# Kernel optimization log

Measured on AMD Instinct MI355X. Metric: run time of the kernel, lower is better.

Reference implementation:

```python
import jax, jax.numpy as jnp
import numpy as np

D_MODEL = 1024
HIDDEN = 512
NUM_EXPERTS = 16
TOP_K = 2
CAP_FACTOR = 1.25
ALPHA = 0.01


def setup_inputs() -> dict:
    key = jax.random.key(0)
    ks = jax.random.split(key, 10)
    s_in = 1.0 / np.sqrt(D_MODEL)
    s_h = 1.0 / np.sqrt(HIDDEN)
    return {
        "x": jax.random.normal(ks[0], (4, 4096, D_MODEL), dtype=jnp.float32),
        "gate_w": jax.random.normal(ks[1], (D_MODEL, NUM_EXPERTS), dtype=jnp.float32) * s_in,
        "gate_b": jnp.zeros((NUM_EXPERTS,), dtype=jnp.float32),
        "gp_w": jax.random.normal(ks[2], (NUM_EXPERTS, D_MODEL, HIDDEN), dtype=jnp.float32) * s_in,
        "gp_b": jnp.zeros((NUM_EXPERTS, HIDDEN), dtype=jnp.float32),
        "up_w": jax.random.normal(ks[3], (NUM_EXPERTS, D_MODEL, HIDDEN), dtype=jnp.float32) * s_in,
        "up_b": jnp.zeros((NUM_EXPERTS, HIDDEN), dtype=jnp.float32),
        "dp_w": jax.random.normal(ks[4], (NUM_EXPERTS, HIDDEN, D_MODEL), dtype=jnp.float32) * s_h,
        "dp_b": jnp.zeros((NUM_EXPERTS, D_MODEL), dtype=jnp.float32),
    }


def reference(x, gate_w, gate_b, gp_w, gp_b, up_w, up_b, dp_w, dp_b):
    B, S, D = x.shape
    T = B * S
    xf = x.reshape(T, D)

    # --- MoEGate ---
    logits = xf @ gate_w + gate_b                      # [T, E]
    scores = jax.nn.softmax(logits, axis=-1)
    topk_w, topk_i = jax.lax.top_k(scores, TOP_K)      # [T, K]
    # norm_topk_prob=True in DeepSeekMoE
    topk_w = topk_w / (jnp.sum(topk_w, axis=-1, keepdims=True) + 1e-9)

    one_hot = jax.nn.one_hot(topk_i, NUM_EXPERTS, dtype=jnp.float32)  # [T, K, E]
    load = jnp.sum(one_hot, axis=(0, 1))               # [E]
    capacity = CAP_FACTOR * (T * TOP_K) / NUM_EXPERTS
    capacity_penalty = jnp.sum(jax.nn.relu(load - capacity)) / NUM_EXPERTS / T
    aux_loss = ALPHA * capacity_penalty

    # combine weight of expert e for each token: [T, E]
    comb = jnp.einsum("tke,tk->te", one_hot, topk_w)

    # --- dispatch/combine (dense per-expert, weighted by comb) ---
    out = jnp.zeros_like(xf)
    for e in range(NUM_EXPERTS):
        # Expert: down_proj(gate_proj(x) * silu(up_proj(x)))
        h = (xf @ gp_w[e] + gp_b[e]) * jax.nn.silu(xf @ up_w[e] + up_b[e])
        y = h @ dp_w[e] + dp_b[e]
        out = out + comb[:, e:e + 1] * y

    return out.reshape(B, S, D), aux_loss
```

## Files before the change

### kernel.cpp

```cpp
#include <hip/hip_runtime.h>
#include <hip/hip_bf16.h>
#include <math.h>

#define T_TOK 16384
#define DMODEL 1024
#define HID 512
#define NEXP 16
#define NASSIGN (T_TOK * 2)
#define HIST_BLK 64
#define TOK_PER_BLK (T_TOK / HIST_BLK)
#define NMB_MAX 143

typedef __bf16 bf16_8 __attribute__((ext_vector_type(8)));
typedef __bf16 bf16_4 __attribute__((ext_vector_type(4)));
typedef float f32_4 __attribute__((ext_vector_type(4)));

__device__ __forceinline__ void gload16(const __bf16* g, __bf16* l) {
  __builtin_amdgcn_global_load_lds(
      (const __attribute__((address_space(1))) void*)g,
      (__attribute__((address_space(3))) void*)l, 16, 0, 0);
}

__global__ __launch_bounds__(256) void gate_compute_kernel(
    const float* __restrict__ x, const float* __restrict__ gw, const float* __restrict__ gb,
    __bf16* __restrict__ xb, int* __restrict__ topk_idx, float2* __restrict__ topk_w)
{
  __shared__ __align__(16) float gws[4 * 1024 * 4];

  int tid = threadIdx.x;
#pragma unroll
  for (int i = 0; i < 16; ++i) {
    int c = i * 256 + tid;
    f32_4 v = ((const f32_4*)gw)[c];
    ((f32_4*)gws)[((c & 3) << 10) | (c >> 2)] = v;
  }
  __syncthreads();

  int wave = tid >> 6, lane = tid & 63;
  int tbase = blockIdx.x * 32 + wave * 8;

#pragma unroll 1
  for (int pass = 0; pass < 2; ++pass) {
    int t0 = tbase + pass * 4;
    const float* xr0 = x + (size_t)t0 * DMODEL;
    const float* xr1 = xr0 + DMODEL;
    const float* xr2 = xr1 + DMODEL;
    const float* xr3 = xr2 + DMODEL;
    __bf16* xw0 = xb + (size_t)t0 * DMODEL;
    __bf16* xw1 = xw0 + DMODEL;
    __bf16* xw2 = xw1 + DMODEL;
    __bf16* xw3 = xw2 + DMODEL;

    f32_4 acc0[4], acc1[4], acc2[4], acc3[4];
    {
      f32_4 z = {0.f, 0.f, 0.f, 0.f};
#pragma unroll
      for (int g = 0; g < 4; ++g) { acc0[g] = z; acc1[g] = z; acc2[g] = z; acc3[g] = z; }
    }

#pragma unroll
    for (int j = 0; j < 16; ++j) {
      int k = j * 64 + lane;
      float xv0 = xr0[k], xv1 = xr1[k], xv2 = xr2[k], xv3 = xr3[k];
      xw0[k] = (__bf16)xv0;
      xw1[k] = (__bf16)xv1;
      xw2[k] = (__bf16)xv2;
      xw3[k] = (__bf16)xv3;
      f32_4 w0 = ((const f32_4*)gws)[k];
      f32_4 w1 = ((const f32_4*)gws)[1024 + k];
      f32_4 w2 = ((const f32_4*)gws)[2048 + k];
      f32_4 w3 = ((const f32_4*)gws)[3072 + k];
      acc0[0] += xv0 * w0; acc0[1] += xv0 * w1; acc0[2] += xv0 * w2; acc0[3] += xv0 * w3;
      acc1[0] += xv1 * w0; acc1[1] += xv1 * w1; acc1[2] += xv1 * w2; acc1[3] += xv1 * w3;
      acc2[0] += xv2 * w0; acc2[1] += xv2 * w1; acc2[2] += xv2 * w2; acc2[3] += xv2 * w3;
      acc3[0] += xv3 * w0; acc3[1] += xv3 * w1; acc3[2] += xv3 * w2; acc3[3] += xv3 * w3;
    }

#pragma unroll
    for (int g = 0; g < 4; ++g)
#pragma unroll
      for (int w = 0; w < 4; ++w) {
        float v0 = acc0[g][w], v1 = acc1[g][w], v2 = acc2[g][w], v3 = acc3[g][w];
#pragma unroll
        for (int s = 32; s; s >>= 1) {
          v0 += __shfl_xor(v0, s, 64);
          v1 += __shfl_xor(v1, s, 64);
          v2 += __shfl_xor(v2, s, 64);
          v3 += __shfl_xor(v3, s, 64);
        }
        acc0[g][w] = v0; acc1[g][w] = v1; acc2[g][w] = v2; acc3[g][w] = v3;
      }

    int ti = lane & 3;
    float sc[16];
#pragma unroll
    for (int e = 0; e < 16; ++e) {
      int g = e >> 2, w = e & 3;
      float v = ti == 0 ? acc0[g][w] : ti == 1 ? acc1[g][w] : ti == 2 ? acc2[g][w] : acc3[g][w];
      sc[e] = v + gb[e];
    }
    float mx = -1e30f;
#pragma unroll
    for (int e = 0; e < 16; ++e) mx = fmaxf(mx, sc[e]);
    float Z = 0.f;
#pragma unroll
    for (int e = 0; e < 16; ++e) { sc[e] = expf(sc[e] - mx); Z += sc[e]; }
    int i0 = 0; float s0 = sc[0];
#pragma unroll
    for (int e = 1; e < 16; ++e) if (sc[e] > s0) { s0 = sc[e]; i0 = e; }
    int i1 = -1; float s1 = -1e30f;
#pragma unroll
    for (int e = 0; e < 16; ++e) if (e != i0 && sc[e] > s1) { s1 = sc[e]; i1 = e; }
    s0 /= Z; s1 /= Z;
    float dn = s0 + s1 + 1e-9f;
    if (lane < 4) {
      int t = t0 + ti;
      topk_idx[t] = i0 | (i1 << 8);
      topk_w[t] = make_float2(s0 / dn, s1 / dn);
    }
  }
}

__global__ __launch_bounds__(256) void hist_kernel(
    const int* __restrict__ topk_idx, int* __restrict__ block_hist)
{
  __shared__ int cnt[NEXP];
  int tid = threadIdx.x;
  if (tid < NEXP) cnt[tid] = 0;
  __syncthreads();
  int t = blockIdx.x * TOK_PER_BLK + tid;
  int p = topk_idx[t];
  atomicAdd(&cnt[p & 0xff], 1);
  atomicAdd(&cnt[p >> 8], 1);
  __syncthreads();
  if (tid < NEXP) block_hist[blockIdx.x * NEXP + tid] = cnt[tid];
}

__global__ void scan2_kernel(const int* __restrict__ block_hist,
                             int* __restrict__ counts, int* __restrict__ offsets,
                             int* __restrict__ block_base, int* __restrict__ mb_tab,
                             int* __restrict__ nmb, float* __restrict__ aux_out)
{
  __shared__ int cl[NEXP];
  int lane = threadIdx.x;
  if (lane < NEXP) {
    int s = 0;
    for (int b = 0; b < HIST_BLK; ++b) s += block_hist[b * NEXP + lane];
    cl[lane] = s;
    counts[lane] = s;
  }
  __syncthreads();
  if (lane < NEXP) {
    int off = 0;
    for (int e = 0; e < lane; ++e) off += cl[e];
    offsets[lane] = off;
    int base = off;
    for (int b = 0; b < HIST_BLK; ++b) {
      block_base[b * NEXP + lane] = base;
      base += block_hist[b * NEXP + lane];
    }
  }
  if (lane == 0) {
    int tot = 0; float pen = 0.f;
    const float cap = 1.25f * (float)(T_TOK * 2) / (float)NEXP;
    for (int e = 0; e < NEXP; ++e) {
      tot += cl[e];
      float ld = (float)cl[e] - cap;
      pen += ld > 0.f ? ld : 0.f;
    }
    offsets[NEXP] = tot;
    aux_out[0] = 0.01f * pen / (float)NEXP / (float)T_TOK;
    int idx = 0;
    for (int e = 0; e < NEXP; ++e) {
      int nb = (cl[e] + 255) >> 8;
      for (int b = 0; b < nb; ++b) mb_tab[idx++] = (e << 8) | b;
    }
    nmb[0] = idx;
  }
}

__global__ __launch_bounds__(256) void scatter_kernel(
    const int* __restrict__ topk_idx, const int* __restrict__ block_base,
    int* __restrict__ tok_list, int2* __restrict__ tok_slots)
{
  __shared__ int base[NEXP];
  int tid = threadIdx.x;
  if (tid < NEXP) base[tid] = block_base[blockIdx.x * NEXP + tid];
  __syncthreads();
  int t = blockIdx.x * TOK_PER_BLK + tid;
  int p = topk_idx[t];
  int i0 = p & 0xff, i1 = p >> 8;
  int p0 = atomicAdd(&base[i0], 1);
  tok_list[p0] = t;
  int p1 = atomicAdd(&base[i1], 1);
  tok_list[p1] = t;
  tok_slots[t] = make_int2(p0, p1);
}

__global__ __launch_bounds__(256) void transpose_w1_kernel(const float* __restrict__ gp,
                                                           const float* __restrict__ up,
                                                           __bf16* __restrict__ wb1)
{
  __shared__ float tile[32][33];
  int ez = blockIdx.z;
  int e = ez >> 1, isup = ez & 1;
  const float* in = isup ? up : gp;
  int c0 = blockIdx.x * 32, r0 = blockIdx.y * 32;
  const float* src = in + ((size_t)e * 1024 + r0) * 512 + c0;
#pragma unroll
  for (int i = 0; i < 4; ++i) {
    int r = threadIdx.y + i * 8;
    tile[r][threadIdx.x] = src[(size_t)r * 512 + threadIdx.x];
  }
  __syncthreads();
#pragma unroll
  for (int i = 0; i < 4; ++i) {
    int cc = threadIdx.y + i * 8;
    int np = 2 * c0 + 2 * (cc & ~15) + (cc & 15) + 16 * isup;
    wb1[((size_t)e * 1024 + np) * 1024 + r0 + threadIdx.x] = (__bf16)tile[threadIdx.x][cc];
  }
}

__global__ __launch_bounds__(256) void transpose_dp_kernel(const float* __restrict__ in,
                                                           __bf16* __restrict__ out)
{
  __shared__ float tile[32][33];
  int e = blockIdx.z;
  int c0 = blockIdx.x * 32, r0 = blockIdx.y * 32;
  const float* src = in + ((size_t)e * 512 + r0) * 1024 + c0;
#pragma unroll
  for (int i = 0; i < 4; ++i) {
    int r = threadIdx.y + i * 8;
    tile[r][threadIdx.x] = src[(size_t)r * 1024 + threadIdx.x];
  }
  __syncthreads();
  __bf16* dst = out + ((size_t)e * 1024 + c0) * 512 + r0;
#pragma unroll
  for (int i = 0; i < 4; ++i) {
    int c = threadIdx.y + i * 8;
    dst[(size_t)c * 512 + threadIdx.x] = (__bf16)tile[threadIdx.x][c];
  }
}


#define PHASE_MID()                                          \
  __builtin_amdgcn_sched_barrier(0);                         \
  __builtin_amdgcn_s_barrier();                              \
  asm volatile("s_waitcnt lgkmcnt(0)" ::: "memory");         \
  __builtin_amdgcn_sched_barrier(0);                         \
  __builtin_amdgcn_s_setprio(1);

#define PHASE_END()                                          \
  __builtin_amdgcn_s_setprio(0);                             \
  __builtin_amdgcn_sched_barrier(0);                         \
  __builtin_amdgcn_s_barrier();

#define MF(mi, ni, a, b) acc[mi][ni] = __builtin_amdgcn_mfma_f32_16x16x32_bf16(a, b, acc[mi][ni], 0, 0, 0)

#define STAGE_A(b, kt) {                                       \
    gload16(ga0 + (kt) * 32, lds + (b) * 16384 + tid * 8);     \
    gload16(ga1 + (kt) * 32, lds + (b) * 16384 + 4096 + tid * 8); }
#define STAGE_B(b, kt) {                                       \
    gload16(gb0 + (kt) * 32, lds + (b) * 16384 + 8192 + tid * 8); \
    gload16(gb1 + (kt) * 32, lds + (b) * 16384 + 12288 + tid * 8); }

#define GTILE(ktv, STG, ENDVM)                                                    \
  {                                                                               \
    const __bf16* A_ = lds + ((ktv) & 3) * 16384;                                 \
    const __bf16* B_ = A_ + 8192;                                                 \
    bf16_8 af0, af1, af2, af3, bf0, bf1, bf2, bf3;                                \
    af0 = *(const bf16_8*)(A_ + abase + 0 * 512 + aq);                            \
    af1 = *(const bf16_8*)(A_ + abase + 1 * 512 + aq);                            \
    af2 = *(const bf16_8*)(A_ + abase + 2 * 512 + aq);                            \
    af3 = *(const bf16_8*)(A_ + abase + 3 * 512 + aq);                            \
    bf0 = *(const bf16_8*)(B_ + bbase + 0 * 512 + aq);                            \
    bf1 = *(const bf16_8*)(B_ + bbase + 1 * 512 + aq);                            \
    bf2 = *(const bf16_8*)(B_ + bbase + 2 * 512 + aq);                            \
    bf3 = *(const bf16_8*)(B_ + bbase + 3 * 512 + aq);                            \
    if (STG) STAGE_A(((ktv) + 3) & 3, (ktv) + 3);                                 \
    PHASE_MID();                                                                  \
    MF(0, 0, af0, bf0); MF(0, 1, af0, bf1); MF(0, 2, af0, bf2); MF(0, 3, af0, bf3); \
    MF(1, 0, af1, bf0); MF(1, 1, af1, bf1); MF(1, 2, af1, bf2); MF(1, 3, af1, bf3); \
    MF(2, 0, af2, bf0); MF(2, 1, af2, bf1); MF(2, 2, af2, bf2); MF(2, 3, af2, bf3); \
    MF(3, 0, af3, bf0); MF(3, 1, af3, bf1); MF(3, 2, af3, bf2); MF(3, 3, af3, bf3); \
    PHASE_END();                                                                  \
    af0 = *(const bf16_8*)(A_ + abase + 4 * 512 + aq);                            \
    af1 = *(const bf16_8*)(A_ + abase + 5 * 512 + aq);                            \
    af2 = *(const bf16_8*)(A_ + abase + 6 * 512 + aq);                            \
    af3 = *(const bf16_8*)(A_ + abase + 7 * 512 + aq);                            \
    if (STG) STAGE_B(((ktv) + 3) & 3, (ktv) + 3);                                 \
    PHASE_MID();                                                                  \
    MF(4, 0, af0, bf0); MF(4, 1, af0, bf1); MF(4, 2, af0, bf2); MF(4, 3, af0, bf3); \
    MF(5, 0, af1, bf0); MF(5, 1, af1, bf1); MF(5, 2, af1, bf2); MF(5, 3, af1, bf3); \
    MF(6, 0, af2, bf0); MF(6, 1, af2, bf1); MF(6, 2, af2, bf2); MF(6, 3, af2, bf3); \
    MF(7, 0, af3, bf0); MF(7, 1, af3, bf1); MF(7, 2, af3, bf2); MF(7, 3, af3, bf3); \
    __builtin_amdgcn_s_setprio(0);                                                \
    __builtin_amdgcn_sched_barrier(0);                                            \
    if ((ENDVM) == 8)      asm volatile("s_waitcnt vmcnt(8)" ::: "memory");       \
    else if ((ENDVM) == 4) asm volatile("s_waitcnt vmcnt(4)" ::: "memory");       \
    else if ((ENDVM) == 0) asm volatile("s_waitcnt vmcnt(0)" ::: "memory");       \
    __builtin_amdgcn_sched_barrier(0);                                            \
    __builtin_amdgcn_s_barrier();                                                 \
  }

template<int KTILES>
__device__ __forceinline__ void gemm8w(
    const __bf16* ga0, const __bf16* ga1,
    const __bf16* gb0, const __bf16* gb1,
    __bf16* lds, f32_4 (&acc)[8][4])
{
  const int tid = threadIdx.x;
  const int wid = tid >> 6, wr = wid >> 2, wc = wid & 3;
  const int lane = tid & 63, quad = lane >> 4, l16 = lane & 15;
  const int aq = (quad ^ (l16 & 3)) * 8;
  const int abase = (wr * 128 + l16) * 32;
  const int bbase = (wc * 64 + l16) * 32;

  STAGE_A(0, 0); STAGE_B(0, 0);
  STAGE_A(1, 1); STAGE_B(1, 1);
  STAGE_A(2, 2); STAGE_B(2, 2);
  asm volatile("s_waitcnt vmcnt(8)" ::: "memory");
  __builtin_amdgcn_sched_barrier(0);
  __builtin_amdgcn_s_barrier();

#pragma unroll 1
  for (int kt = 0; kt < KTILES - 3; ++kt) {
    GTILE(kt, 1, 8);
  }
  GTILE(KTILES - 3, 0, 4);
  GTILE(KTILES - 2, 0, 0);
  GTILE(KTILES - 1, 0, -1);
}

__global__ __launch_bounds__(512, 2) void ffn1_kernel(
    const __bf16* __restrict__ xb, const __bf16* __restrict__ wb1,
    const float* __restrict__ gp_b, const float* __restrict__ up_b,
    const int* __restrict__ counts, const int* __restrict__ offsets,
    const int* __restrict__ tok_list, const int* __restrict__ mb_tab,
    const int* __restrict__ nmb, __bf16* __restrict__ h)
{
  __shared__ __align__(16) __bf16 lds[4 * 16384];
  __shared__ int toks[256];

  int lin = blockIdx.y * 4 + blockIdx.x;
  int xcd = lin & 7, sub = lin >> 3;
  int wg = (xcd < 4 ? xcd * 72 : 288 + (xcd - 4) * 71) + sub;
  int y = wg >> 2, xn = wg & 3;
  if (y >= nmb[0]) return;
  int me = mb_tab[y];
  int e = me >> 8;
  int m0 = (me & 255) << 8;
  int cnt = counts[e], offe = offsets[e];
  int n0 = xn * 256;

  int tid = threadIdx.x;
  if (tid < 256) {
    int r = m0 + tid;
    toks[tid] = tok_list[offe + (r < cnt ? r : cnt - 1)];
  }
  __syncthreads();

  int rr = tid >> 2;
  int ko = ((tid & 3) ^ (rr & 3)) * 8;

  const __bf16* ga0 = xb + (size_t)toks[rr] * DMODEL + ko;
  const __bf16* ga1 = xb + (size_t)toks[128 + rr] * DMODEL + ko;
  const __bf16* gb0 = wb1 + ((size_t)e * 1024 + n0 + rr) * DMODEL + ko;
  const __bf16* gb1 = wb1 + ((size_t)e * 1024 + n0 + 128 + rr) * DMODEL + ko;

  f32_4 acc[8][4];
  {
    f32_4 z = {0.f, 0.f, 0.f, 0.f};
#pragma unroll
    for (int a = 0; a < 8; ++a)
#pragma unroll
      for (int b = 0; b < 4; ++b) acc[a][b] = z;
  }

  gemm8w<DMODEL / 32>(ga0, ga1, gb0, gb1, lds, acc);

  int wid = tid >> 6, wr = wid >> 2, wc = wid & 3;
  int lane = tid & 63, quad = lane >> 4, l16 = lane & 15;

#pragma unroll
  for (int mi = 0; mi < 8; ++mi)
#pragma unroll
    for (int j = 0; j < 2; ++j) {
      int c = (n0 >> 1) + wc * 32 + j * 16 + l16;
      float gbias = gp_b[e * HID + c];
      float ubias = up_b[e * HID + c];
#pragma unroll
      for (int rg = 0; rg < 4; ++rg) {
        int r = m0 + wr * 128 + mi * 16 + quad * 4 + rg;
        if (r < cnt) {
          float g = acc[mi][2 * j][rg] + gbias;
          float u = acc[mi][2 * j + 1][rg] + ubias;
          float sw = u / (1.f + expf(-u));
          h[(size_t)(offe + r) * HID + c] = (__bf16)(g * sw);
        }
      }
    }
}

__global__ __launch_bounds__(512, 2) void ffn2_kernel(
    const __bf16* __restrict__ h, const __bf16* __restrict__ dpb, const float* __restrict__ dp_b,
    const int* __restrict__ counts, const int* __restrict__ offsets,
    const int* __restrict__ mb_tab, const int* __restrict__ nmb,
    __bf16* __restrict__ ybuf)
{
  __shared__ __align__(16) __bf16 lds[4 * 16384];

  int lin = blockIdx.y * 4 + blockIdx.x;
  int xcd = lin & 7, sub = lin >> 3;
  int wg = (xcd < 4 ? xcd * 72 : 288 + (xcd - 4) * 71) + sub;
  int y = wg >> 2, xn = wg & 3;
  if (y >= nmb[0]) return;
  int me = mb_tab[y];
  int e = me >> 8;
  int m0 = (me & 255) << 8;
  int cnt = counts[e], offe = offsets[e];
  int n0 = xn * 256;

  int tid = threadIdx.x;
  int rr = tid >> 2;
  int ko = ((tid & 3) ^ (rr & 3)) * 8;

  int ra0 = m0 + rr;        if (ra0 >= cnt) ra0 = cnt - 1;
  int ra1 = m0 + 128 + rr;  if (ra1 >= cnt) ra1 = cnt - 1;
  const __bf16* ga0 = h + (size_t)(offe + ra0) * HID + ko;
  const __bf16* ga1 = h + (size_t)(offe + ra1) * HID + ko;
  const __bf16* gb0 = dpb + ((size_t)e * DMODEL + n0 + rr) * HID + ko;
  const __bf16* gb1 = dpb + ((size_t)e * DMODEL + n0 + 128 + rr) * HID + ko;

  f32_4 acc[8][4];
  {
    f32_4 z = {0.f, 0.f, 0.f, 0.f};
#pragma unroll
    for (int a = 0; a < 8; ++a)
#pragma unroll
      for (int b = 0; b < 4; ++b) acc[a][b] = z;
  }

  gemm8w<HID / 32>(ga0, ga1, gb0, gb1, lds, acc);

  int wid = tid >> 6, wr = wid >> 2, wc = wid & 3;
  int lane = tid & 63, quad = lane >> 4, l16 = lane & 15;

#pragma unroll
  for (int mi = 0; mi < 8; ++mi)
#pragma unroll
    for (int ni = 0; ni < 4; ++ni) {
      int n = n0 + wc * 64 + ni * 16 + l16;
      float bias = dp_b[e * DMODEL + n];
#pragma unroll
      for (int rg = 0; rg < 4; ++rg) {
        int r = m0 + wr * 128 + mi * 16 + quad * 4 + rg;
        if (r < cnt) {
          float v = acc[mi][ni][rg] + bias;
          ybuf[(size_t)(offe + r) * DMODEL + n] = (__bf16)v;
        }
      }
    }
}

__global__ __launch_bounds__(256) void combine_kernel(
    const __bf16* __restrict__ ybuf, const int2* __restrict__ tok_slots,
    const float2* __restrict__ topk_w, float* __restrict__ out)
{
  int tid = threadIdx.x;
  int t = blockIdx.x * 2 + (tid >> 7);
  int d = (tid & 127) * 8;
  int2 sl = tok_slots[t];
  float2 w = topk_w[t];
  bf16_8 y0 = *(const bf16_8*)(ybuf + (size_t)sl.x * DMODEL + d);
  bf16_8 y1 = *(const bf16_8*)(ybuf + (size_t)sl.y * DMODEL + d);
  float* o = out + (size_t)t * DMODEL + d;
  f32_4 r0, r1;
#pragma unroll
  for (int i = 0; i < 4; ++i) r0[i] = w.x * (float)y0[i] + w.y * (float)y1[i];
#pragma unroll
  for (int i = 0; i < 4; ++i) r1[i] = w.x * (float)y0[4 + i] + w.y * (float)y1[4 + i];
  *(f32_4*)o = r0;
  *(f32_4*)(o + 4) = r1;
}

extern "C" void kernel_launch(void* const* d_in, const int* in_sizes, int n_in,
                              void* d_out, int out_size, void* d_ws, size_t ws_size,
                              hipStream_t stream)
{
  const float* x      = (const float*)d_in[0];
  const float* gate_w = (const float*)d_in[1];
  const float* gate_b = (const float*)d_in[2];
  const float* gp_w   = (const float*)d_in[3];
  const float* gp_b   = (const float*)d_in[4];
  const float* up_w   = (const float*)d_in[5];
  const float* up_b   = (const float*)d_in[6];
  const float* dp_w   = (const float*)d_in[7];
  const float* dp_b   = (const float*)d_in[8];

  char* ws = (char*)d_ws;
  size_t o = 0;
  __bf16* xb  = (__bf16*)(ws + o); o += (size_t)T_TOK * DMODEL * 2;
  __bf16* wb1 = (__bf16*)(ws + o); o += (size_t)NEXP * 1024 * DMODEL * 2;
  __bf16* dpb = (__bf16*)(ws + o); o += (size_t)NEXP * DMODEL * HID * 2;
  __bf16* hbuf = (__bf16*)(ws + o); o += (size_t)NASSIGN * HID * 2;
  int*   tok_list = (int*)(ws + o); o += (size_t)NASSIGN * 4;
  int2*  tok_slots = (int2*)(ws + o); o += (size_t)T_TOK * 8;
  int*   topk_idx = (int*)(ws + o); o += (size_t)T_TOK * 4;
  float2* topk_w  = (float2*)(ws + o); o += (size_t)T_TOK * 8;
  int*   block_hist = (int*)(ws + o); o += (size_t)HIST_BLK * NEXP * 4;
  int*   block_base = (int*)(ws + o); o += (size_t)HIST_BLK * NEXP * 4;
  int*   counts   = (int*)(ws + o); o += 64;
  int*   offsets  = (int*)(ws + o); o += 128;
  int*   mb_tab   = (int*)(ws + o); o += 4 * 160;
  int*   nmb      = (int*)(ws + o); o += 64;
  __bf16* ybuf = (__bf16*)ws;

  float* out = (float*)d_out;
  float* aux = out + (size_t)T_TOK * DMODEL;

  gate_compute_kernel<<<T_TOK / 32, 256, 0, stream>>>(x, gate_w, gate_b, xb, topk_idx, topk_w);
  hist_kernel<<<HIST_BLK, TOK_PER_BLK, 0, stream>>>(topk_idx, block_hist);
  scan2_kernel<<<1, 64, 0, stream>>>(block_hist, counts, offsets, block_base, mb_tab, nmb, aux);
  scatter_kernel<<<HIST_BLK, TOK_PER_BLK, 0, stream>>>(topk_idx, block_base, tok_list, tok_slots);
  transpose_w1_kernel<<<dim3(512 / 32, 1024 / 32, 2 * NEXP), dim3(32, 8), 0, stream>>>(gp_w, up_w, wb1);
  transpose_dp_kernel<<<dim3(1024 / 32, 512 / 32, NEXP), dim3(32, 8), 0, stream>>>(dp_w, dpb);
  ffn1_kernel<<<dim3(4, NMB_MAX, 1), 512, 0, stream>>>(xb, wb1, gp_b, up_b,
                                                       counts, offsets, tok_list, mb_tab, nmb, hbuf);
  ffn2_kernel<<<dim3(4, NMB_MAX, 1), 512, 0, stream>>>(hbuf, dpb, dp_b,
                                                       counts, offsets, mb_tab, nmb, ybuf);
  combine_kernel<<<T_TOK / 2, 256, 0, stream>>>(ybuf, tok_slots, topk_w, out);
}
```

Before: 486.6 us.

## Switch GEMM pipeline from 4-stage to 2-stage LDS buffering with new swizzle

```diff
diff --git a/kernel.cpp b/kernel.cpp
--- a/kernel.cpp
+++ b/kernel.cpp
@@ -257,38 +257,38 @@
 
 #define MF(mi, ni, a, b) acc[mi][ni] = __builtin_amdgcn_mfma_f32_16x16x32_bf16(a, b, acc[mi][ni], 0, 0, 0)
 
-#define STAGE_A(b, kt) {                                       \
-    gload16(ga0 + (kt) * 32, lds + (b) * 16384 + tid * 8);     \
+#define STAGE_A(b, kt) {                                          \
+    gload16(ga0 + (kt) * 32, lds + (b) * 16384 + tid * 8);        \
     gload16(ga1 + (kt) * 32, lds + (b) * 16384 + 4096 + tid * 8); }
-#define STAGE_B(b, kt) {                                       \
+#define STAGE_B(b, kt) {                                          \
     gload16(gb0 + (kt) * 32, lds + (b) * 16384 + 8192 + tid * 8); \
     gload16(gb1 + (kt) * 32, lds + (b) * 16384 + 12288 + tid * 8); }
 
-#define GTILE(ktv, STG, ENDVM)                                                    \
+#define GTILE(ktv, STG)                                                           \
   {                                                                               \
-    const __bf16* A_ = lds + ((ktv) & 3) * 16384;                                 \
+    const __bf16* A_ = lds + ((ktv) & 1) * 16384;                                 \
     const __bf16* B_ = A_ + 8192;                                                 \
     bf16_8 af0, af1, af2, af3, bf0, bf1, bf2, bf3;                                \
-    af0 = *(const bf16_8*)(A_ + abase + 0 * 512 + aq);                            \
-    af1 = *(const bf16_8*)(A_ + abase + 1 * 512 + aq);                            \
-    af2 = *(const bf16_8*)(A_ + abase + 2 * 512 + aq);                            \
-    af3 = *(const bf16_8*)(A_ + abase + 3 * 512 + aq);                            \
-    bf0 = *(const bf16_8*)(B_ + bbase + 0 * 512 + aq);                            \
-    bf1 = *(const bf16_8*)(B_ + bbase + 1 * 512 + aq);                            \
-    bf2 = *(const bf16_8*)(B_ + bbase + 2 * 512 + aq);                            \
-    bf3 = *(const bf16_8*)(B_ + bbase + 3 * 512 + aq);                            \
-    if (STG) STAGE_A(((ktv) + 3) & 3, (ktv) + 3);                                 \
+    af0 = *(const bf16_8*)(A_ + abase + 0 * 512 + sq);                            \
+    af1 = *(const bf16_8*)(A_ + abase + 1 * 512 + sq);                            \
+    af2 = *(const bf16_8*)(A_ + abase + 2 * 512 + sq);                            \
+    af3 = *(const bf16_8*)(A_ + abase + 3 * 512 + sq);                            \
+    bf0 = *(const bf16_8*)(B_ + bbase + 0 * 512 + sq);                            \
+    bf1 = *(const bf16_8*)(B_ + bbase + 1 * 512 + sq);                            \
+    bf2 = *(const bf16_8*)(B_ + bbase + 2 * 512 + sq);                            \
+    bf3 = *(const bf16_8*)(B_ + bbase + 3 * 512 + sq);                            \
+    if (STG) STAGE_A(((ktv) + 1) & 1, (ktv) + 1);                                 \
     PHASE_MID();                                                                  \
     MF(0, 0, af0, bf0); MF(0, 1, af0, bf1); MF(0, 2, af0, bf2); MF(0, 3, af0, bf3); \
     MF(1, 0, af1, bf0); MF(1, 1, af1, bf1); MF(1, 2, af1, bf2); MF(1, 3, af1, bf3); \
     MF(2, 0, af2, bf0); MF(2, 1, af2, bf1); MF(2, 2, af2, bf2); MF(2, 3, af2, bf3); \
     MF(3, 0, af3, bf0); MF(3, 1, af3, bf1); MF(3, 2, af3, bf2); MF(3, 3, af3, bf3); \
     PHASE_END();                                                                  \
-    af0 = *(const bf16_8*)(A_ + abase + 4 * 512 + aq);                            \
-    af1 = *(const bf16_8*)(A_ + abase + 5 * 512 + aq);                            \
-    af2 = *(const bf16_8*)(A_ + abase + 6 * 512 + aq);                            \
-    af3 = *(const bf16_8*)(A_ + abase + 7 * 512 + aq);                            \
-    if (STG) STAGE_B(((ktv) + 3) & 3, (ktv) + 3);                                 \
+    af0 = *(const bf16_8*)(A_ + abase + 4 * 512 + sq);                            \
+    af1 = *(const bf16_8*)(A_ + abase + 5 * 512 + sq);                            \
+    af2 = *(const bf16_8*)(A_ + abase + 6 * 512 + sq);                            \
+    af3 = *(const bf16_8*)(A_ + abase + 7 * 512 + sq);                            \
+    if (STG) STAGE_B(((ktv) + 1) & 1, (ktv) + 1);                                 \
     PHASE_MID();                                                                  \
     MF(4, 0, af0, bf0); MF(4, 1, af0, bf1); MF(4, 2, af0, bf2); MF(4, 3, af0, bf3); \
     MF(5, 0, af1, bf0); MF(5, 1, af1, bf1); MF(5, 2, af1, bf2); MF(5, 3, af1, bf3); \
@@ -296,9 +296,7 @@
     MF(7, 0, af3, bf0); MF(7, 1, af3, bf1); MF(7, 2, af3, bf2); MF(7, 3, af3, bf3); \
     __builtin_amdgcn_s_setprio(0);                                                \
     __builtin_amdgcn_sched_barrier(0);                                            \
-    if ((ENDVM) == 8)      asm volatile("s_waitcnt vmcnt(8)" ::: "memory");       \
-    else if ((ENDVM) == 4) asm volatile("s_waitcnt vmcnt(4)" ::: "memory");       \
-    else if ((ENDVM) == 0) asm volatile("s_waitcnt vmcnt(0)" ::: "memory");       \
+    if (STG) { asm volatile("s_waitcnt vmcnt(0)" ::: "memory"); }                 \
     __builtin_amdgcn_sched_barrier(0);                                            \
     __builtin_amdgcn_s_barrier();                                                 \
   }
@@ -312,24 +310,20 @@
   const int tid = threadIdx.x;
   const int wid = tid >> 6, wr = wid >> 2, wc = wid & 3;
   const int lane = tid & 63, quad = lane >> 4, l16 = lane & 15;
-  const int aq = (quad ^ (l16 & 3)) * 8;
+  const int sq = (quad ^ ((l16 >> 1) & 3)) * 8;
   const int abase = (wr * 128 + l16) * 32;
   const int bbase = (wc * 64 + l16) * 32;
 
   STAGE_A(0, 0); STAGE_B(0, 0);
-  STAGE_A(1, 1); STAGE_B(1, 1);
-  STAGE_A(2, 2); STAGE_B(2, 2);
-  asm volatile("s_waitcnt vmcnt(8)" ::: "memory");
+  asm volatile("s_waitcnt vmcnt(0)" ::: "memory");
   __builtin_amdgcn_sched_barrier(0);
   __builtin_amdgcn_s_barrier();
 
 #pragma unroll 1
-  for (int kt = 0; kt < KTILES - 3; ++kt) {
-    GTILE(kt, 1, 8);
-  }
-  GTILE(KTILES - 3, 0, 4);
-  GTILE(KTILES - 2, 0, 0);
-  GTILE(KTILES - 1, 0, -1);
+  for (int kt = 0; kt < KTILES - 1; ++kt) {
+    GTILE(kt, 1);
+  }
+  GTILE(KTILES - 1, 0);
 }
 
 __global__ __launch_bounds__(512, 2) void ffn1_kernel(
@@ -339,7 +333,7 @@
     const int* __restrict__ tok_list, const int* __restrict__ mb_tab,
     const int* __restrict__ nmb, __bf16* __restrict__ h)
 {
-  __shared__ __align__(16) __bf16 lds[4 * 16384];
+  __shared__ __align__(16) __bf16 lds[2 * 16384];
   __shared__ int toks[256];
 
   int lin = blockIdx.y * 4 + blockIdx.x;
@@ -361,7 +355,7 @@
   __syncthreads();
 
   int rr = tid >> 2;
-  int ko = ((tid & 3) ^ (rr & 3)) * 8;
+  int ko = ((tid & 3) ^ ((rr >> 1) & 3)) * 8;
 
   const __bf16* ga0 = xb + (size_t)toks[rr] * DMODEL + ko;
   const __bf16* ga1 = xb + (size_t)toks[128 + rr] * DMODEL + ko;
@@ -408,7 +402,7 @@
     const int* __restrict__ mb_tab, const int* __restrict__ nmb,
     __bf16* __restrict__ ybuf)
 {
-  __shared__ __align__(16) __bf16 lds[4 * 16384];
+  __shared__ __align__(16) __bf16 lds[2 * 16384];
 
   int lin = blockIdx.y * 4 + blockIdx.x;
   int xcd = lin & 7, sub = lin >> 3;
@@ -423,7 +417,7 @@
 
   int tid = threadIdx.x;
   int rr = tid >> 2;
-  int ko = ((tid & 3) ^ (rr & 3)) * 8;
+  int ko = ((tid & 3) ^ ((rr >> 1) & 3)) * 8;
 
   int ra0 = m0 + rr;        if (ra0 >= cnt) ra0 = cnt - 1;
   int ra1 = m0 + 128 + rr;  if (ra1 >= cnt) ra1 = cnt - 1;
```

Result: no change. 487.5 us (+0.2%).
